# Performance work log

Hardware: AMD Instinct MI355X
Metric: run time of the kernel (lower is better)

## Reference

```python
import jax, jax.numpy as jnp
import numpy as np

C_IN = 256
GROUP = C_IN // 4  # module hard-codes group = C_in/4 -> 4 channels per group
EPS = 1e-5

@jax.custom_vjp
def binarize(x):
    # 1-bit quantization: sign forward, hardtanh straight-through backward
    return jnp.sign(x)

def _bin_fwd(x):
    return jnp.sign(x), x

def _bin_bwd(x, g):
    return (g * (jnp.abs(x) <= 1.0).astype(g.dtype),)

binarize.defvjp(_bin_fwd, _bin_bwd)

def channel_shuffle(x, g):
    # [N,C,H,W] -> [N,g,C/g,H,W] -> [N,C/g,g,H,W] -> [N,C,H,W]
    N, C, H, W = x.shape
    return x.reshape(N, g, C // g, H, W).transpose(0, 2, 1, 3, 4).reshape(N, C, H, W)


def setup_inputs() -> dict:
    key = jax.random.key(0)
    ks = jax.random.split(key, 6)
    x = jax.random.normal(ks[0], (32, C_IN, 56, 56), jnp.float32)
    # grouped conv weight: [C_out, C_in/group, kH, kW] = [256, 4, 3, 3]
    weight = jax.random.normal(ks[1], (C_IN, C_IN // GROUP, 3, 3), jnp.float32) * 0.1
    gamma = 1.0 + 0.1 * jax.random.normal(ks[2], (C_IN,), jnp.float32)
    beta = 0.1 * jax.random.normal(ks[3], (C_IN,), jnp.float32)
    running_mean = 0.1 * jax.random.normal(ks[4], (C_IN,), jnp.float32)
    running_var = jax.random.uniform(ks[5], (C_IN,), jnp.float32, 0.5, 1.5)
    return dict(x=x, weight=weight, gamma=gamma, beta=beta,
                running_mean=running_mean, running_var=running_var)


def reference(x, weight, gamma, beta, running_mean, running_var):
    # BatchNorm2d (inference-mode, affine=True)
    inv = gamma * jax.lax.rsqrt(running_var + EPS)
    xb = x * inv[None, :, None, None] + (beta - running_mean * inv)[None, :, None, None]
    # Conv2d_1w1a: binarize activations and weights, grouped 3x3 conv, no bias
    a = binarize(xb)
    w = binarize(weight)
    out = jax.lax.conv_general_dilated(
        a, w,
        window_strides=(1, 1),
        padding=((1, 1), (1, 1)),
        dimension_numbers=('NCHW', 'OIHW', 'NCHW'),
        feature_group_count=GROUP,
    )
    out = channel_shuffle(out, GROUP)
    # stride == 1 -> shortcut is identity
    return out + x
```

## Files before the change

### kernel.cpp

```cpp
#include <hip/hip_runtime.h>
#include <stdint.h>

#define H 56
#define W 56
#define HW (H * W)
#define CIN 256
#define IMG (CIN * HW)
#define EPS 1e-5f

#define ROWW 8
#define TR2 30
#define TSZ (TR2 * ROWW)
#define ATASKS 406
#define BTASKS 392

__device__ __forceinline__ float mul_rn(float a, float b) {
    float d; asm("v_mul_f32 %0, %1, %2" : "=v"(d) : "v"(a), "v"(b)); return d;
}
__device__ __forceinline__ float add_rn(float a, float b) {
    float d; asm("v_add_f32 %0, %1, %2" : "=v"(d) : "v"(a), "v"(b)); return d;
}
__device__ __forceinline__ float sub_rn(float a, float b) {
    float d; asm("v_sub_f32 %0, %1, %2" : "=v"(d) : "v"(a), "v"(b)); return d;
}
__device__ __forceinline__ float mul_rn_sv(float s, float v) {
    float d; asm("v_mul_f32 %0, %1, %2" : "=v"(d) : "s"(s), "v"(v)); return d;
}
__device__ __forceinline__ float add_rn_sv(float s, float v) {
    float d; asm("v_add_f32 %0, %1, %2" : "=v"(d) : "s"(s), "v"(v)); return d;
}
__device__ __forceinline__ float rfl_f(float x) {
    return __int_as_float(__builtin_amdgcn_readfirstlane(__float_as_int(x)));
}


struct Stage { float4 q[4]; };

__device__ __forceinline__ void issueA(const float* __restrict__ Xn, int g, int half,
                                       int t, Stage& st) {
    int ar = t / 14;
    int cg = t - ar * 14;
    int ir = ar + half * 27;
    const float* base = Xn + (size_t)(g * 4) * HW + ir * W + cg * 4;
#pragma unroll
    for (int ci = 0; ci < 4; ++ci)
        st.q[ci] = *reinterpret_cast<const float4*>(base + (size_t)ci * HW);
}

__device__ __forceinline__ void bn_pack(const Stage& st, const float inv[4], const float bias[4],
                                        uint32_t& s16, uint32_t& z16) {
    s16 = 0u; z16 = 0u;
#pragma unroll
    for (int ci = 0; ci < 4; ++ci) {
        float t0 = add_rn_sv(bias[ci], mul_rn_sv(inv[ci], st.q[ci].x));
        float t1 = add_rn_sv(bias[ci], mul_rn_sv(inv[ci], st.q[ci].y));
        float t2 = add_rn_sv(bias[ci], mul_rn_sv(inv[ci], st.q[ci].z));
        float t3 = add_rn_sv(bias[ci], mul_rn_sv(inv[ci], st.q[ci].w));
        s16 |= ((t0 > 0.f ? 1u : 0u) << ci)        | ((t1 > 0.f ? 1u : 0u) << (4 + ci))
             | ((t2 > 0.f ? 1u : 0u) << (8 + ci))  | ((t3 > 0.f ? 1u : 0u) << (12 + ci));
        z16 |= ((t0 != 0.f ? 1u : 0u) << ci)       | ((t1 != 0.f ? 1u : 0u) << (4 + ci))
             | ((t2 != 0.f ? 1u : 0u) << (8 + ci)) | ((t3 != 0.f ? 1u : 0u) << (12 + ci));
    }
}

__device__ __forceinline__ void convA(const Stage& st, const float inv[4], const float bias[4],
                                      uint32_t* s_t, uint32_t* z_t, int t, int half) {
    int ar = t / 14;
    int cg = t - ar * 14;
    int rt = ar + 1 - half;
    uint32_t s16, z16;
    bn_pack(st, inv, bias, s16, z16);
    reinterpret_cast<uint16_t*>(&s_t[rt * ROWW])[cg] = (uint16_t)s16;
    reinterpret_cast<uint16_t*>(&z_t[rt * ROWW])[cg] = (uint16_t)z16;
}

__device__ __forceinline__ void taskB(const uint32_t* s_t, const uint32_t* z_t,
                                      const float* __restrict__ Xn, float* __restrict__ On,
                                      int g, int half, int task,
                                      const uint32_t wsj[4][3], const uint32_t wzj[4][3],
                                      bool full) {
    int hl = task / 14;
    int cg = task - hl * 14;
    int w0 = cg * 4;

    uint64_t vs[3], vz[3];
    int off;
    if (w0 == 0) {
        off = 0;
#pragma unroll
        for (int r = 0; r < 3; ++r) {
            int base = (hl + r) * ROWW;
            vs[r] = (((uint64_t)s_t[base] | ((uint64_t)s_t[base + 1] << 32)) << 4);
            vz[r] = (((uint64_t)z_t[base] | ((uint64_t)z_t[base + 1] << 32)) << 4);
        }
    } else {
        int st = 4 * w0 - 4;
        int i0 = st >> 5;
        off = st & 31;
#pragma unroll
        for (int r = 0; r < 3; ++r) {
            int base = (hl + r) * ROWW + i0;
            vs[r] = ((uint64_t)s_t[base] | ((uint64_t)s_t[base + 1] << 32));
            vz[r] = ((uint64_t)z_t[base] | ((uint64_t)z_t[base + 1] << 32));
        }
    }

    int res[4][4];
    if (full) {
#pragma unroll
        for (int k = 0; k < 4; ++k) {
            int sh = off + 4 * k;
            uint32_t s0 = (uint32_t)(vs[0] >> sh) & 0xFFFu;
            uint32_t s1 = (uint32_t)(vs[1] >> sh) & 0xFFFu;
            uint32_t s2 = (uint32_t)(vs[2] >> sh) & 0xFFFu;
            uint32_t z0 = (uint32_t)(vz[0] >> sh) & 0xFFFu;
            uint32_t z1 = (uint32_t)(vz[1] >> sh) & 0xFFFu;
            uint32_t z2 = (uint32_t)(vz[2] >> sh) & 0xFFFu;
            int vb = __popc(z0) + __popc(z1) + __popc(z2);
#pragma unroll
            for (int j = 0; j < 4; ++j) {
                int pc = __popc((s0 ^ wsj[j][0]) & z0)
                       + __popc((s1 ^ wsj[j][1]) & z1)
                       + __popc((s2 ^ wsj[j][2]) & z2);
                res[j][k] = vb - 2 * pc;
            }
        }
    } else {
#pragma unroll
        for (int k = 0; k < 4; ++k) {
            int sh = off + 4 * k;
            uint32_t s0 = (uint32_t)(vs[0] >> sh) & 0xFFFu;
            uint32_t s1 = (uint32_t)(vs[1] >> sh) & 0xFFFu;
            uint32_t s2 = (uint32_t)(vs[2] >> sh) & 0xFFFu;
            uint32_t z0 = (uint32_t)(vz[0] >> sh) & 0xFFFu;
            uint32_t z1 = (uint32_t)(vz[1] >> sh) & 0xFFFu;
            uint32_t z2 = (uint32_t)(vz[2] >> sh) & 0xFFFu;
#pragma unroll
            for (int j = 0; j < 4; ++j) {
                uint32_t m0 = z0 & wzj[j][0];
                uint32_t m1 = z1 & wzj[j][1];
                uint32_t m2 = z2 & wzj[j][2];
                int vb = __popc(m0) + __popc(m1) + __popc(m2);
                int pc = __popc((s0 ^ wsj[j][0]) & m0)
                       + __popc((s1 ^ wsj[j][1]) & m1)
                       + __popc((s2 ^ wsj[j][2]) & m2);
                res[j][k] = vb - 2 * pc;
            }
        }
    }

    size_t pbase = (size_t)(half * 28 + hl) * W + w0;
    float4 sc[4];
#pragma unroll
    for (int j = 0; j < 4; ++j)
        sc[j] = *reinterpret_cast<const float4*>(Xn + (size_t)(j * 64 + g) * HW + pbase);
#pragma unroll
    for (int j = 0; j < 4; ++j) {
        size_t cofs = (size_t)(j * 64 + g) * HW + pbase;
        float4 o;
        o.x = add_rn((float)res[j][0], sc[j].x);
        o.y = add_rn((float)res[j][1], sc[j].y);
        o.z = add_rn((float)res[j][2], sc[j].z);
        o.w = add_rn((float)res[j][3], sc[j].w);
        *reinterpret_cast<float4*>(On + cofs) = o;
    }
}

__global__ __launch_bounds__(256, 8)
void binconv_kernel(const float* __restrict__ X,
                    const float* __restrict__ Wt,
                    const float* __restrict__ gamma,
                    const float* __restrict__ beta,
                    const float* __restrict__ mean,
                    const float* __restrict__ var,
                    float* __restrict__ out, int nHalf) {
    __shared__ uint32_t s_tile[2][TSZ];
    __shared__ uint32_t z_tile[2][TSZ];
    __shared__ uint32_t ws_l[4][3];
    __shared__ uint32_t wz_l[4][3];

    const int bx   = blockIdx.x;
    const int half = bx & 1;
    const int g    = (bx >> 1) & 63;
    const int n0   = bx >> 7;
    const int tid  = threadIdx.x;

    for (int i = tid; i < 2 * TSZ; i += 256) {
        (&s_tile[0][0])[i] = 0u;
        (&z_tile[0][0])[i] = 0u;
    }

    const float* Xn0 = X   + (size_t)n0 * IMG;
    const float* Xn1 = X   + (size_t)(n0 + nHalf) * IMG;
    float*       On0 = out + (size_t)n0 * IMG;
    float*       On1 = out + (size_t)(n0 + nHalf) * IMG;

    Stage a0, a1;
    issueA(Xn0, g, half, tid, a0);
    if (tid < ATASKS - 256) issueA(Xn0, g, half, tid + 256, a1);

    if (tid < 4) {
        const float* wc = Wt + (size_t)(g * 4 + tid) * 36;
        for (int r = 0; r < 3; ++r) {
            uint32_t s = 0, z = 0;
            for (int ci = 0; ci < 4; ++ci)
                for (int kw = 0; kw < 3; ++kw) {
                    float v = wc[ci * 9 + r * 3 + kw];
                    int b = kw * 4 + ci;
                    s |= (v > 0.f  ? 1u : 0u) << b;
                    z |= (v != 0.f ? 1u : 0u) << b;
                }
            ws_l[tid][r] = s; wz_l[tid][r] = z;
        }
    }

    float inv[4], bias[4];
#pragma unroll
    for (int ci = 0; ci < 4; ++ci) {
        int c = g * 4 + ci;
        float s  = sqrtf(var[c] + EPS);
        float r  = 1.0f / s;
        float iv = mul_rn(gamma[c], r);
        inv[ci]  = rfl_f(iv);
        bias[ci] = rfl_f(sub_rn(beta[c], mul_rn(mean[c], iv)));
    }

    __syncthreads();

    convA(a0, inv, bias, s_tile[0], z_tile[0], tid, half);
    if (tid < ATASKS - 256) convA(a1, inv, bias, s_tile[0], z_tile[0], tid + 256, half);

    uint32_t wsj[4][3], wzj[4][3];
    bool full = true;
#pragma unroll
    for (int j = 0; j < 4; ++j)
#pragma unroll
        for (int r = 0; r < 3; ++r) {
            wsj[j][r] = __builtin_amdgcn_readfirstlane(ws_l[j][r]);
            wzj[j][r] = __builtin_amdgcn_readfirstlane(wz_l[j][r]);
            full = full && (wzj[j][r] == 0xFFFu);
        }

    __syncthreads();

    issueA(Xn1, g, half, tid, a0);
    __builtin_amdgcn_sched_barrier(0);

    taskB(s_tile[0], z_tile[0], Xn0, On0, g, half, tid, wsj, wzj, full);

    convA(a0, inv, bias, s_tile[1], z_tile[1], tid, half);
    if (tid < ATASKS - 256) issueA(Xn1, g, half, tid + 256, a1);
    __builtin_amdgcn_sched_barrier(0);

    if (tid < BTASKS - 256)
        taskB(s_tile[0], z_tile[0], Xn0, On0, g, half, tid + 256, wsj, wzj, full);

    if (tid < ATASKS - 256) convA(a1, inv, bias, s_tile[1], z_tile[1], tid + 256, half);

    __syncthreads();

    taskB(s_tile[1], z_tile[1], Xn1, On1, g, half, tid, wsj, wzj, full);
    if (tid < BTASKS - 256)
        taskB(s_tile[1], z_tile[1], Xn1, On1, g, half, tid + 256, wsj, wzj, full);
}

extern "C" void kernel_launch(void* const* d_in, const int* in_sizes, int n_in,
                              void* d_out, int out_size, void* d_ws, size_t ws_size,
                              hipStream_t stream) {
    const float* X     = (const float*)d_in[0];
    const float* Wt    = (const float*)d_in[1];
    const float* gamma = (const float*)d_in[2];
    const float* beta  = (const float*)d_in[3];
    const float* mean  = (const float*)d_in[4];
    const float* var   = (const float*)d_in[5];
    float* out = (float*)d_out;

    int N     = in_sizes[0] / IMG;
    int nHalf = N >> 1;

    binconv_kernel<<<nHalf * 64 * 2, 256, 0, stream>>>(X, Wt, gamma, beta, mean, var, out, nHalf);
}
```

Baseline: 220.9 us.

## Pipeline two row-halves of one image per block instead of two images

Each block now handles one (image, group) pair and pipelines its top and bottom row halves through the double-buffered bit tiles, where before it handled one half of two different images. The grid size stays the same, and the per-block weight and BN setup is now shared across both halves of a single image, which may improve cache locality on the overlapping halo rows. The launch-bounds occupancy hint also drops from 8 to 6 blocks, giving the compiler more registers but possibly fewer resident waves.

```diff
diff --git a/kernel.cpp b/kernel.cpp
--- a/kernel.cpp
+++ b/kernel.cpp
@@ -36,11 +36,11 @@
 
 struct Stage { float4 q[4]; };
 
-__device__ __forceinline__ void issueA(const float* __restrict__ Xn, int g, int half,
+__device__ __forceinline__ void issueA(const float* __restrict__ Xn, int g, int rowbase,
                                        int t, Stage& st) {
     int ar = t / 14;
     int cg = t - ar * 14;
-    int ir = ar + half * 27;
+    int ir = rowbase + ar;
     const float* base = Xn + (size_t)(g * 4) * HW + ir * W + cg * 4;
 #pragma unroll
     for (int ci = 0; ci < 4; ++ci)
@@ -64,10 +64,10 @@
 }
 
 __device__ __forceinline__ void convA(const Stage& st, const float inv[4], const float bias[4],
-                                      uint32_t* s_t, uint32_t* z_t, int t, int half) {
+                                      uint32_t* s_t, uint32_t* z_t, int t, int rtoff) {
     int ar = t / 14;
     int cg = t - ar * 14;
-    int rt = ar + 1 - half;
+    int rt = ar + rtoff;
     uint32_t s16, z16;
     bn_pack(st, inv, bias, s16, z16);
     reinterpret_cast<uint16_t*>(&s_t[rt * ROWW])[cg] = (uint16_t)s16;
@@ -166,38 +166,35 @@
     }
 }
 
-__global__ __launch_bounds__(256, 8)
+__global__ __launch_bounds__(256, 6)
 void binconv_kernel(const float* __restrict__ X,
                     const float* __restrict__ Wt,
                     const float* __restrict__ gamma,
                     const float* __restrict__ beta,
                     const float* __restrict__ mean,
                     const float* __restrict__ var,
-                    float* __restrict__ out, int nHalf) {
+                    float* __restrict__ out) {
     __shared__ uint32_t s_tile[2][TSZ];
     __shared__ uint32_t z_tile[2][TSZ];
     __shared__ uint32_t ws_l[4][3];
     __shared__ uint32_t wz_l[4][3];
 
-    const int bx   = blockIdx.x;
-    const int half = bx & 1;
-    const int g    = (bx >> 1) & 63;
-    const int n0   = bx >> 7;
-    const int tid  = threadIdx.x;
+    const int bx  = blockIdx.x;
+    const int n   = bx >> 6;
+    const int g   = bx & 63;
+    const int tid = threadIdx.x;
 
     for (int i = tid; i < 2 * TSZ; i += 256) {
         (&s_tile[0][0])[i] = 0u;
         (&z_tile[0][0])[i] = 0u;
     }
 
-    const float* Xn0 = X   + (size_t)n0 * IMG;
-    const float* Xn1 = X   + (size_t)(n0 + nHalf) * IMG;
-    float*       On0 = out + (size_t)n0 * IMG;
-    float*       On1 = out + (size_t)(n0 + nHalf) * IMG;
+    const float* Xn = X   + (size_t)n * IMG;
+    float*       On = out + (size_t)n * IMG;
 
     Stage a0, a1;
-    issueA(Xn0, g, half, tid, a0);
-    if (tid < ATASKS - 256) issueA(Xn0, g, half, tid + 256, a1);
+    issueA(Xn, g, 0, tid, a0);
+    if (tid < ATASKS - 256) issueA(Xn, g, 0, tid + 256, a1);
 
     if (tid < 4) {
         const float* wc = Wt + (size_t)(g * 4 + tid) * 36;
@@ -227,8 +224,8 @@
 
     __syncthreads();
 
-    convA(a0, inv, bias, s_tile[0], z_tile[0], tid, half);
-    if (tid < ATASKS - 256) convA(a1, inv, bias, s_tile[0], z_tile[0], tid + 256, half);
+    convA(a0, inv, bias, s_tile[0], z_tile[0], tid, 1);
+    if (tid < ATASKS - 256) convA(a1, inv, bias, s_tile[0], z_tile[0], tid + 256, 1);
 
     uint32_t wsj[4][3], wzj[4][3];
     bool full = true;
@@ -243,25 +240,25 @@
 
     __syncthreads();
 
-    issueA(Xn1, g, half, tid, a0);
+    issueA(Xn, g, 27, tid, a0);
     __builtin_amdgcn_sched_barrier(0);
 
-    taskB(s_tile[0], z_tile[0], Xn0, On0, g, half, tid, wsj, wzj, full);
-
-    convA(a0, inv, bias, s_tile[1], z_tile[1], tid, half);
-    if (tid < ATASKS - 256) issueA(Xn1, g, half, tid + 256, a1);
+    taskB(s_tile[0], z_tile[0], Xn, On, g, 0, tid, wsj, wzj, full);
+
+    convA(a0, inv, bias, s_tile[1], z_tile[1], tid, 0);
+    if (tid < ATASKS - 256) issueA(Xn, g, 27, tid + 256, a1);
     __builtin_amdgcn_sched_barrier(0);
 
     if (tid < BTASKS - 256)
-        taskB(s_tile[0], z_tile[0], Xn0, On0, g, half, tid + 256, wsj, wzj, full);
-
-    if (tid < ATASKS - 256) convA(a1, inv, bias, s_tile[1], z_tile[1], tid + 256, half);
+        taskB(s_tile[0], z_tile[0], Xn, On, g, 0, tid + 256, wsj, wzj, full);
+
+    if (tid < ATASKS - 256) convA(a1, inv, bias, s_tile[1], z_tile[1], tid + 256, 0);
 
     __syncthreads();
 
-    taskB(s_tile[1], z_tile[1], Xn1, On1, g, half, tid, wsj, wzj, full);
+    taskB(s_tile[1], z_tile[1], Xn, On, g, 1, tid, wsj, wzj, full);
     if (tid < BTASKS - 256)
-        taskB(s_tile[1], z_tile[1], Xn1, On1, g, half, tid + 256, wsj, wzj, full);
+        taskB(s_tile[1], z_tile[1], Xn, On, g, 1, tid + 256, wsj, wzj, full);
 }
 
 extern "C" void kernel_launch(void* const* d_in, const int* in_sizes, int n_in,
@@ -275,8 +272,7 @@
     const float* var   = (const float*)d_in[5];
     float* out = (float*)d_out;
 
-    int N     = in_sizes[0] / IMG;
-    int nHalf = N >> 1;
-
-    binconv_kernel<<<nHalf * 64 * 2, 256, 0, stream>>>(X, Wt, gamma, beta, mean, var, out, nHalf);
-}
+    int N = in_sizes[0] / IMG;
+
+    binconv_kernel<<<N * 64, 256, 0, stream>>>(X, Wt, gamma, beta, mean, var, out);
+}
```

Result: faster. 211.0 us (-4.5%).
